# Performance work log

Measured on AMD Instinct MI355X. Metric: run time of the kernel, lower is better.

The kernel has to match this reference:

```python
import jax, jax.numpy as jnp
import numpy as np

EPS = 1e-3  # keras LayerNormalization default epsilon

def layernorm(x, gamma, beta):
    mu = jnp.mean(x, axis=-1, keepdims=True)
    var = jnp.var(x, axis=-1, keepdims=True)
    return (x - mu) * jax.lax.rsqrt(var + EPS) * gamma + beta

def setup_inputs() -> dict:
    key = jax.random.key(0)
    ks = jax.random.split(key, 20)
    B, N, T, Dimg, H = 512, 100, 14, 2048, 768
    s = lambda k, *sh: jax.random.normal(k, sh, dtype=jnp.float32) * 0.02
    return {
        "img_feat": jax.random.normal(ks[0], (B, N, Dimg), dtype=jnp.float32),
        "ques_feat": jax.random.normal(ks[1], (B, T, H), dtype=jnp.float32),
        "Wc": s(ks[2], Dimg, H), "bc": jnp.zeros((H,), jnp.float32),
        "Wq": s(ks[3], H, H),    "bq": jnp.zeros((H,), jnp.float32),
        "Wi": s(ks[4], Dimg, H), "bi": jnp.zeros((H,), jnp.float32),
        "wqa": s(ks[5], H, 1), "bqa": jnp.zeros((1,), jnp.float32),
        "wia": s(ks[6], H, 1), "bia": jnp.zeros((1,), jnp.float32),
        "g1": jnp.ones((N,), jnp.float32), "b1": jnp.zeros((N,), jnp.float32),
        "g2": jnp.ones((H,), jnp.float32), "b2": jnp.zeros((H,), jnp.float32),
        "g3": jnp.ones((T,), jnp.float32), "b3": jnp.zeros((T,), jnp.float32),
        "g4": jnp.ones((H,), jnp.float32), "b4": jnp.zeros((H,), jnp.float32),
        "g5": jnp.ones((N,), jnp.float32), "b5": jnp.zeros((N,), jnp.float32),
    }

def reference(img_feat, ques_feat, Wc, bc, Wq, bq, Wi, bi, wqa, bqa, wia, bia,
              g1, b1, g2, b2, g3, b3, g4, b4, g5, b5):
    # img_feat: [B,N,Dimg], ques_feat: [B,T,H]
    img_corr = img_feat @ Wc + bc                                   # [B,N,H]
    wm = jnp.einsum('bth,bnh->btn', ques_feat, img_corr)            # [B,T,N]
    wm = jax.nn.relu(layernorm(wm, g1, b1))
    ques_embed = ques_feat @ Wq + bq                                # [B,T,H]
    img_embed = img_feat @ Wi + bi                                  # [B,N,H]
    transform_img = jnp.einsum('btn,bnh->bth', wm, img_embed)       # [B,T,H]
    ques_atten_sum = jax.nn.relu(layernorm(transform_img + ques_embed, g2, b2))
    # dropout is identity at inference
    ques_atten = (ques_atten_sum @ wqa + bqa)[..., 0]               # [B,T]
    ques_atten = jax.nn.softmax(layernorm(ques_atten, g3, b3), axis=-1)
    transform_ques = jnp.einsum('btn,bth->bnh', wm, ques_embed)     # [B,N,H]
    img_atten_sum = jax.nn.relu(layernorm(transform_ques + img_embed, g4, b4))
    img_atten = (img_atten_sum @ wia + bia)[..., 0]                 # [B,N]
    img_atten = jax.nn.softmax(layernorm(img_atten, g5, b5), axis=-1)
    ques_atten_feat = jnp.einsum('bt,bth->bh', ques_atten, ques_feat)  # [B,H]
    img_atten_feat = jnp.einsum('bn,bnd->bd', img_atten, img_feat)     # [B,Dimg]
    return (img_atten_feat, ques_atten_feat)
```

## Files before the change

### kernel.cpp

```cpp
#include <hip/hip_runtime.h>

using f32x4     = __attribute__((ext_vector_type(4))) float;
using bf16x8    = __attribute__((ext_vector_type(8))) short;
using ushort8_t = __attribute__((ext_vector_type(8))) unsigned short;

__device__ __forceinline__ unsigned short f2bf(float f) {
    unsigned u = __builtin_bit_cast(unsigned, f);
    u += 0x7fffu + ((u >> 16) & 1u);
    return (unsigned short)(u >> 16);
}
__device__ __forceinline__ float bf2f(unsigned short h) {
    return __builtin_bit_cast(float, (unsigned)h << 16);
}

__device__ __forceinline__ float wave_sum(float v) {
#pragma unroll
    for (int off = 32; off > 0; off >>= 1) v += __shfl_xor(v, off, 64);
    return v;
}
__device__ __forceinline__ float wave_max(float v) {
#pragma unroll
    for (int off = 32; off > 0; off >>= 1) v = fmaxf(v, __shfl_xor(v, off, 64));
    return v;
}

#define GLP(p)  ((const __attribute__((address_space(1))) void*)(p))
#define LDSP(p) ((__attribute__((address_space(3))) void*)(p))

__global__ __launch_bounds__(256) void cvt_bf16(const float* __restrict__ in,
                                                unsigned short* __restrict__ out, long n8) {
    long i = (long)blockIdx.x * 256 + threadIdx.x;
    long stride = (long)gridDim.x * 256;
    for (; i < n8; i += stride) {
        const float4* p = (const float4*)(in + i * 8);
        float4 a = p[0], b = p[1];
        ushort8_t v;
        v[0] = f2bf(a.x); v[1] = f2bf(a.y); v[2] = f2bf(a.z); v[3] = f2bf(a.w);
        v[4] = f2bf(b.x); v[5] = f2bf(b.y); v[6] = f2bf(b.z); v[7] = f2bf(b.w);
        *(ushort8_t*)(out + i * 8) = v;
    }
}

__global__ void pack_w(const float* __restrict__ Wc, const float* __restrict__ Wi,
                       unsigned short* __restrict__ Wp) {
    int n = blockIdx.x, k = blockIdx.y * 256 + threadIdx.x;
    float v = (n < 768) ? Wc[(size_t)k * 768 + n] : Wi[(size_t)k * 768 + (n - 768)];
    Wp[(size_t)n * 2048 + k] = f2bf(v);
}

__global__ void pack_wq(const float* __restrict__ Wq, unsigned short* __restrict__ Wqt) {
    int n = blockIdx.x, k = blockIdx.y * 256 + threadIdx.x;
    Wqt[(size_t)n * 768 + k] = f2bf(Wq[(size_t)k * 768 + n]);
}

template <int OUTBF>
__global__ __launch_bounds__(512, 1) void gemm8(
    const unsigned short* __restrict__ A, const unsigned short* __restrict__ Bt,
    const float* __restrict__ bias0, const float* __restrict__ bias1, int nsplit,
    void* __restrict__ Cv, int N, int K, int NTN)
{
    __shared__ unsigned short LA[2][2][8192];
    __shared__ unsigned short LB[2][2][8192];
    const int tid = threadIdx.x, lane = tid & 63, wid = tid >> 6;

    int nwg = (int)gridDim.x, bid = (int)blockIdx.x;
    if ((nwg & 7) == 0) { int cpx = nwg >> 3; bid = (bid & 7) * cpx + (bid >> 3); }
    const int tn = bid % NTN, tm = bid / NTN;
    const size_t m0 = (size_t)tm * 256, n0 = (size_t)tn * 256;
    const int NT = K >> 6;
    const int NIT = NT >> 1;

    const int wr = wid >> 2, wc = wid & 3;
    const int hb = wc >> 1;
    const int fr = lane & 15, fs = lane >> 4;

    const int r0 = tid >> 3, s0 = ((tid & 7) - r0) & 7;
    const int r1 = r0 + 64,  s1 = ((tid & 7) - r1) & 7;
    const unsigned short* pA[2][2];
    const unsigned short* pB[2][2];
#pragma unroll
    for (int h = 0; h < 2; ++h) {
        pA[h][0] = A  + (m0 + h * 128 + r0) * K + s0 * 8;
        pA[h][1] = A  + (m0 + h * 128 + r1) * K + s1 * 8;
        pB[h][0] = Bt + (n0 + h * 128 + r0) * K + s0 * 8;
        pB[h][1] = Bt + (n0 + h * 128 + r1) * K + s1 * 8;
    }
    const int d0 = tid * 8, d1 = (tid + 512) * 8;

#define STG_A(h, t, B_) do { \
    __builtin_amdgcn_global_load_lds(GLP(pA[h][0] + (size_t)(t) * 64), LDSP(&LA[B_][h][d0]), 16, 0, 0); \
    __builtin_amdgcn_global_load_lds(GLP(pA[h][1] + (size_t)(t) * 64), LDSP(&LA[B_][h][d1]), 16, 0, 0); \
} while (0)
#define STG_B(h, t, B_) do { \
    __builtin_amdgcn_global_load_lds(GLP(pB[h][0] + (size_t)(t) * 64), LDSP(&LB[B_][h][d0]), 16, 0, 0); \
    __builtin_amdgcn_global_load_lds(GLP(pB[h][1] + (size_t)(t) * 64), LDSP(&LB[B_][h][d1]), 16, 0, 0); \
} while (0)

    int offA[2][4], offB[2][2];
#pragma unroll
    for (int mq = 0; mq < 2; ++mq)
#pragma unroll
        for (int mfl = 0; mfl < 4; ++mfl) {
            int r = mq * 64 + mfl * 16 + fr;
            offA[mq][mfl] = r * 64 + ((fs + r) & 7) * 8;
        }
#pragma unroll
    for (int nq = 0; nq < 2; ++nq)
#pragma unroll
        for (int nfl = 0; nfl < 2; ++nfl) {
            int r = (wc & 1) * 64 + nq * 32 + nfl * 16 + fr;
            offB[nq][nfl] = r * 64 + ((fs + r) & 7) * 8;
        }

#define LDA_SUB(B_, mq) do { \
    _Pragma("unroll") \
    for (int mfl = 0; mfl < 4; ++mfl) { \
        av[mfl][0] = *(const bf16x8*)&LA[B_][wr][offA[mq][mfl]]; \
        av[mfl][1] = *(const bf16x8*)&LA[B_][wr][offA[mq][mfl] ^ 32]; \
    } } while (0)
#define LDB_SUB(B_, nq, bv) do { \
    _Pragma("unroll") \
    for (int nfl = 0; nfl < 2; ++nfl) { \
        bv[nfl][0] = *(const bf16x8*)&LB[B_][hb][offB[nq][nfl]]; \
        bv[nfl][1] = *(const bf16x8*)&LB[B_][hb][offB[nq][nfl] ^ 32]; \
    } } while (0)
#define MMA_Q(mq, nq, bv) do { \
    _Pragma("unroll") \
    for (int ks = 0; ks < 2; ++ks) \
    _Pragma("unroll") \
    for (int mfl = 0; mfl < 4; ++mfl) \
    _Pragma("unroll") \
    for (int nfl = 0; nfl < 2; ++nfl) \
        acc[mq * 4 + mfl][nq * 2 + nfl] = __builtin_amdgcn_mfma_f32_16x16x32_bf16( \
            av[mfl][ks], bv[nfl][ks], acc[mq * 4 + mfl][nq * 2 + nfl], 0, 0, 0); \
    } while (0)
#define BAR  __builtin_amdgcn_s_barrier()
#define SCB  __builtin_amdgcn_sched_barrier(0)
#define LGKM0 do { asm volatile("s_waitcnt lgkmcnt(0)" ::: "memory"); SCB; } while (0)
#define PRIO1 __builtin_amdgcn_s_setprio(1)
#define PRIO0 __builtin_amdgcn_s_setprio(0)

    f32x4 acc[8][4];
#pragma unroll
    for (int i = 0; i < 8; ++i)
#pragma unroll
        for (int j = 0; j < 4; ++j) acc[i][j] = (f32x4){0.f, 0.f, 0.f, 0.f};

    STG_A(0, 0, 0); STG_A(1, 0, 0); STG_B(0, 0, 0); STG_B(1, 0, 0);
    STG_B(0, 1, 1); STG_B(1, 1, 1); STG_A(0, 1, 1);
    asm volatile("s_waitcnt vmcnt(6)" ::: "memory");
    SCB; BAR;

    for (int i = 0; i < NIT; ++i) {
        const int t0 = 2 * i, t1 = 2 * i + 1;
        const bool st = (i + 1 < NIT);
        bf16x8 av[4][2], bv0[2][2], bv1[2][2];

        LDA_SUB(0, 0); LDB_SUB(0, 0, bv0);
        STG_A(1, t1, 1);
        BAR; LGKM0;
        PRIO1; MMA_Q(0, 0, bv0); PRIO0;
        BAR;
        LDB_SUB(0, 1, bv1);
        BAR; LGKM0;
        PRIO1; MMA_Q(0, 1, bv1); PRIO0;
        BAR;
        LDA_SUB(0, 1);
        if (st) STG_B(0, t0 + 2, 0);
        BAR; LGKM0;
        PRIO1; MMA_Q(1, 1, bv1); PRIO0;
        BAR;
        if (st) { STG_B(1, t0 + 2, 0); STG_A(0, t0 + 2, 0); }
        BAR;
        PRIO1; MMA_Q(1, 0, bv0); PRIO0;
        if (st) asm volatile("s_waitcnt vmcnt(6)" ::: "memory");
        else    asm volatile("s_waitcnt vmcnt(0)" ::: "memory");
        SCB; BAR;
        LDA_SUB(1, 0); LDB_SUB(1, 0, bv0);
        if (st) STG_A(1, t0 + 2, 0);
        BAR; LGKM0;
        PRIO1; MMA_Q(0, 0, bv0); PRIO0;
        BAR;
        LDB_SUB(1, 1, bv1);
        BAR; LGKM0;
        PRIO1; MMA_Q(0, 1, bv1); PRIO0;
        BAR;
        LDA_SUB(1, 1);
        if (st) STG_B(0, t1 + 2, 1);
        BAR; LGKM0;
        PRIO1; MMA_Q(1, 1, bv1); PRIO0;
        BAR;
        if (st) { STG_B(1, t1 + 2, 1); STG_A(0, t1 + 2, 1); }
        BAR;
        PRIO1; MMA_Q(1, 0, bv0); PRIO0;
        if (st) asm volatile("s_waitcnt vmcnt(6)" ::: "memory");
        else    asm volatile("s_waitcnt vmcnt(0)" ::: "memory");
        SCB; BAR;
    }

#undef STG_A
#undef STG_B
#undef LDA_SUB
#undef LDB_SUB
#undef MMA_Q
#undef BAR
#undef SCB
#undef LGKM0
#undef PRIO1
#undef PRIO0

    const int wm = wr * 128, wn = wc * 64;
#pragma unroll
    for (int nf = 0; nf < 4; ++nf) {
        int col = (int)n0 + wn + nf * 16 + fr;
        float bs = (col < nsplit) ? bias0[col] : bias1[col - nsplit];
#pragma unroll
        for (int mf = 0; mf < 8; ++mf) {
            size_t rowb = m0 + wm + mf * 16 + fs * 4;
#pragma unroll
            for (int r = 0; r < 4; ++r) {
                float v = acc[mf][nf][r] + bs;
                if (OUTBF) ((unsigned short*)Cv)[(rowb + r) * N + col] = f2bf(v);
                else       ((float*)Cv)[(rowb + r) * N + col] = v;
            }
        }
    }
}

__global__ __launch_bounds__(256) void fused_kernel(
    const float* __restrict__ qf_g, const unsigned short* __restrict__ qbf,
    const float* __restrict__ qe_g, const unsigned short* __restrict__ imgCE,
    const unsigned short* __restrict__ imf_bf,
    const float* __restrict__ g1, const float* __restrict__ b1,
    const float* __restrict__ g2, const float* __restrict__ b2,
    const float* __restrict__ g3, const float* __restrict__ b3,
    const float* __restrict__ g4, const float* __restrict__ b4,
    const float* __restrict__ g5, const float* __restrict__ b5,
    const float* __restrict__ wqa, const float* __restrict__ bqa,
    const float* __restrict__ wia, const float* __restrict__ bia,
    float* __restrict__ out_i, float* __restrict__ out_q)
{
    const int b = blockIdx.x, tid = threadIdx.x, lane = tid & 63, wid = tid >> 6;
    __shared__ float buf[14 * 768];
    __shared__ float wms[14 * 100];
    __shared__ float red[4][28];
    __shared__ float mu_s[14], rs_s[14], qa_s[14], qw_s[14];
    __shared__ float mu2_s[10], rs2_s[10];
    __shared__ float ia_s[100], iw_s[100];

    {
        const ushort8_t* src = (const ushort8_t*)(qbf + (size_t)b * 14 * 768);
        for (int i = tid; i < 14 * 768 / 8; i += 256) {
            ushort8_t v = src[i];
#pragma unroll
            for (int j = 0; j < 8; ++j) buf[i * 8 + j] = bf2f(v[j]);
        }
    }
    __syncthreads();
    for (int n = wid; n < 100; n += 4) {
        const unsigned short* row = imgCE + ((size_t)b * 100 + n) * 1536;
        float r[12];
#pragma unroll
        for (int j = 0; j < 12; ++j) r[j] = bf2f(row[lane + 64 * j]);
        for (int t = 0; t < 14; ++t) {
            const float* q = buf + t * 768;
            float s = 0.f;
#pragma unroll
            for (int j = 0; j < 12; ++j) s = fmaf(r[j], q[lane + 64 * j], s);
            s = wave_sum(s);
            if (lane == 0) wms[t * 100 + n] = s;
        }
    }
    __syncthreads();
    for (int t = wid; t < 14; t += 4) {
        float x0 = wms[t * 100 + lane];
        float x1 = (lane + 64 < 100) ? wms[t * 100 + lane + 64] : 0.f;
        float s = wave_sum(x0 + x1);
        float q = wave_sum(x0 * x0 + x1 * x1);
        float mu = s * (1.f / 100.f);
        float var = q * (1.f / 100.f) - mu * mu;
        float rs = rsqrtf(var + 1e-3f);
        {
            float v = (x0 - mu) * rs * g1[lane] + b1[lane];
            wms[t * 100 + lane] = v > 0.f ? v : 0.f;
        }
        if (lane + 64 < 100) {
            float v = (x1 - mu) * rs * g1[lane + 64] + b1[lane + 64];
            wms[t * 100 + lane + 64] = v > 0.f ? v : 0.f;
        }
    }
    {
        const float4* src = (const float4*)(qe_g + (size_t)b * 14 * 768);
        for (int i = tid; i < 14 * 768 / 4; i += 256) ((float4*)buf)[i] = src[i];
    }
    __syncthreads();

    {
        float a0[14], a1[14], a2[14];
#pragma unroll
        for (int t = 0; t < 14; ++t) { a0[t] = 0.f; a1[t] = 0.f; a2[t] = 0.f; }

        const unsigned short* ie_base = imgCE + (size_t)b * 100 * 1536 + 768;
        for (int n = 0; n < 100; ++n) {
            const unsigned short* ie = ie_base + (size_t)n * 1536;
            float e0 = bf2f(ie[tid]), e1 = bf2f(ie[tid + 256]), e2 = bf2f(ie[tid + 512]);
#pragma unroll
            for (int t = 0; t < 14; ++t) {
                float w = wms[t * 100 + n];
                a0[t] = fmaf(w, e0, a0[t]); a1[t] = fmaf(w, e1, a1[t]); a2[t] = fmaf(w, e2, a2[t]);
            }
        }
#pragma unroll
        for (int t = 0; t < 14; ++t) {
            a0[t] += buf[t * 768 + tid];
            a1[t] += buf[t * 768 + tid + 256];
            a2[t] += buf[t * 768 + tid + 512];
        }
#pragma unroll
        for (int t = 0; t < 14; ++t) {
            float s = wave_sum(a0[t] + a1[t] + a2[t]);
            float q = wave_sum(a0[t] * a0[t] + a1[t] * a1[t] + a2[t] * a2[t]);
            if (lane == 0) { red[wid][t] = s; red[wid][14 + t] = q; }
        }
        __syncthreads();
        if (tid < 14) {
            float s = red[0][tid] + red[1][tid] + red[2][tid] + red[3][tid];
            float q = red[0][14 + tid] + red[1][14 + tid] + red[2][14 + tid] + red[3][14 + tid];
            float mu = s * (1.f / 768.f);
            float var = q * (1.f / 768.f) - mu * mu;
            mu_s[tid] = mu; rs_s[tid] = rsqrtf(var + 1e-3f);
        }
        __syncthreads();

        float ga = g2[tid], ba = b2[tid], gb = g2[tid + 256], bb = b2[tid + 256],
              gc = g2[tid + 512], bc_ = b2[tid + 512];
        float w0 = wqa[tid], w1 = wqa[tid + 256], w2 = wqa[tid + 512];
#pragma unroll
        for (int t = 0; t < 14; ++t) {
            float mu = mu_s[t], rs = rs_s[t];
            float v0 = fmaxf((a0[t] - mu) * rs * ga + ba, 0.f);
            float v1 = fmaxf((a1[t] - mu) * rs * gb + bb, 0.f);
            float v2 = fmaxf((a2[t] - mu) * rs * gc + bc_, 0.f);
            float p = wave_sum(v0 * w0 + v1 * w1 + v2 * w2);
            if (lane == 0) red[wid][t] = p;
        }
        __syncthreads();
        if (tid < 14) qa_s[tid] = red[0][tid] + red[1][tid] + red[2][tid] + red[3][tid] + bqa[0];
        __syncthreads();
        if (tid == 0) {
            float s = 0.f;
            for (int t = 0; t < 14; ++t) s += qa_s[t];
            float mu = s * (1.f / 14.f);
            float q = 0.f;
            for (int t = 0; t < 14; ++t) { float d = qa_s[t] - mu; q += d * d; }
            float rs = rsqrtf(q * (1.f / 14.f) + 1e-3f);
            float e[14], mx = -1e30f;
            for (int t = 0; t < 14; ++t) { e[t] = (qa_s[t] - mu) * rs * g3[t] + b3[t]; mx = fmaxf(mx, e[t]); }
            float se = 0.f;
            for (int t = 0; t < 14; ++t) { e[t] = expf(e[t] - mx); se += e[t]; }
            float inv = 1.f / se;
            for (int t = 0; t < 14; ++t) qw_s[t] = e[t] * inv;
        }
        __syncthreads();

        const float* qf = qf_g + (size_t)b * 14 * 768;
#pragma unroll
        for (int c = 0; c < 3; ++c) {
            int h = tid + c * 256;
            float o = 0.f;
#pragma unroll
            for (int t = 0; t < 14; ++t) o = fmaf(qw_s[t], qf[t * 768 + h], o);
            out_q[(size_t)b * 768 + h] = o;
        }
    }
    __syncthreads();

    {
        float g4a = g4[tid], b4a = b4[tid], g4b = g4[tid + 256], b4b = b4[tid + 256],
              g4c = g4[tid + 512], b4c = b4[tid + 512];
        float wa = wia[tid], wb = wia[tid + 256], wc_ = wia[tid + 512];

        for (int g = 0; g < 10; ++g) {
            float t0[10], t1[10], t2[10];
#pragma unroll
            for (int i = 0; i < 10; ++i) { t0[i] = 0.f; t1[i] = 0.f; t2[i] = 0.f; }
#pragma unroll
            for (int t = 0; t < 14; ++t) {
                float q0 = buf[t * 768 + tid], q1 = buf[t * 768 + tid + 256], q2 = buf[t * 768 + tid + 512];
#pragma unroll
                for (int i = 0; i < 10; ++i) {
                    float w = wms[t * 100 + g * 10 + i];
                    t0[i] = fmaf(w, q0, t0[i]); t1[i] = fmaf(w, q1, t1[i]); t2[i] = fmaf(w, q2, t2[i]);
                }
            }
#pragma unroll
            for (int i = 0; i < 10; ++i) {
                const unsigned short* ie = imgCE + ((size_t)b * 100 + g * 10 + i) * 1536 + 768;
                t0[i] += bf2f(ie[tid]); t1[i] += bf2f(ie[tid + 256]); t2[i] += bf2f(ie[tid + 512]);
                float s = wave_sum(t0[i] + t1[i] + t2[i]);
                float q = wave_sum(t0[i] * t0[i] + t1[i] * t1[i] + t2[i] * t2[i]);
                if (lane == 0) { red[wid][i] = s; red[wid][10 + i] = q; }
            }
            __syncthreads();
            if (tid < 10) {
                float s = red[0][tid] + red[1][tid] + red[2][tid] + red[3][tid];
                float q = red[0][10 + tid] + red[1][10 + tid] + red[2][10 + tid] + red[3][10 + tid];
                float mu = s * (1.f / 768.f);
                float var = q * (1.f / 768.f) - mu * mu;
                mu2_s[tid] = mu; rs2_s[tid] = rsqrtf(var + 1e-3f);
            }
            __syncthreads();
#pragma unroll
            for (int i = 0; i < 10; ++i) {
                float mu = mu2_s[i], rs = rs2_s[i];
                float v0 = fmaxf((t0[i] - mu) * rs * g4a + b4a, 0.f);
                float v1 = fmaxf((t1[i] - mu) * rs * g4b + b4b, 0.f);
                float v2 = fmaxf((t2[i] - mu) * rs * g4c + b4c, 0.f);
                float p = wave_sum(v0 * wa + v1 * wb + v2 * wc_);
                if (lane == 0) red[wid][i] = p;
            }
            __syncthreads();
            if (tid < 10) ia_s[g * 10 + tid] = red[0][tid] + red[1][tid] + red[2][tid] + red[3][tid] + bia[0];
            __syncthreads();
        }

        if (wid == 0) {
            float x0 = ia_s[lane];
            float x1 = (lane + 64 < 100) ? ia_s[lane + 64] : 0.f;
            float s = wave_sum(x0 + x1);
            float q = wave_sum(x0 * x0 + x1 * x1);
            float mu = s * 0.01f;
            float var = q * 0.01f - mu * mu;
            float rs = rsqrtf(var + 1e-3f);
            float v0 = (x0 - mu) * rs * g5[lane] + b5[lane];
            float v1 = (lane + 64 < 100) ? (x1 - mu) * rs * g5[lane + 64] + b5[lane + 64] : -1e30f;
            float mx = wave_max(fmaxf(v0, v1));
            float e0 = expf(v0 - mx);
            float e1 = (lane + 64 < 100) ? expf(v1 - mx) : 0.f;
            float se = wave_sum(e0 + e1);
            float inv = 1.f / se;
            iw_s[lane] = e0 * inv;
            if (lane + 64 < 100) iw_s[lane + 64] = e1 * inv;
        }
        __syncthreads();

        const unsigned short* imf = imf_bf + (size_t)b * 100 * 2048;
        float acc8[8];
#pragma unroll
        for (int j = 0; j < 8; ++j) acc8[j] = 0.f;
        for (int n = 0; n < 100; ++n) {
            ushort8_t v = *(const ushort8_t*)(imf + (size_t)n * 2048 + tid * 8);
            float w = iw_s[n];
#pragma unroll
            for (int j = 0; j < 8; ++j) acc8[j] = fmaf(w, bf2f(v[j]), acc8[j]);
        }
        float4* dst = (float4*)(out_i + (size_t)b * 2048);
        float4 oA = {acc8[0], acc8[1], acc8[2], acc8[3]};
        float4 oB = {acc8[4], acc8[5], acc8[6], acc8[7]};
        dst[tid * 2] = oA; dst[tid * 2 + 1] = oB;
    }
}

extern "C" void kernel_launch(void* const* d_in, const int* in_sizes, int n_in,
                              void* d_out, int out_size, void* d_ws, size_t ws_size,
                              hipStream_t stream)
{
    const float* img_feat = (const float*)d_in[0];
    const float* ques_feat = (const float*)d_in[1];
    const float* Wc = (const float*)d_in[2];
    const float* bc = (const float*)d_in[3];
    const float* Wq = (const float*)d_in[4];
    const float* bq = (const float*)d_in[5];
    const float* Wi = (const float*)d_in[6];
    const float* bi = (const float*)d_in[7];
    const float* wqa = (const float*)d_in[8];
    const float* bqa = (const float*)d_in[9];
    const float* wia = (const float*)d_in[10];
    const float* bia = (const float*)d_in[11];
    const float* g1 = (const float*)d_in[12]; const float* b1 = (const float*)d_in[13];
    const float* g2 = (const float*)d_in[14]; const float* b2 = (const float*)d_in[15];
    const float* g3 = (const float*)d_in[16]; const float* b3 = (const float*)d_in[17];
    const float* g4 = (const float*)d_in[18]; const float* b4 = (const float*)d_in[19];
    const float* g5 = (const float*)d_in[20]; const float* b5 = (const float*)d_in[21];

    const size_t SZ_WP   = 1536u * 2048u * 2u;
    const size_t SZ_WQT  = 768u * 768u * 2u;
    const size_t SZ_IMG  = 51200ull * 1536u * 2u;
    const size_t SZ_QE   = 7168u * 768u * 4u;
    const size_t SZ_WM   = 512u * 1400u * 4u;
    const size_t SZ_ABF  = 51200ull * 2048u * 2u;
    const size_t SZ_QBF  = 7168u * 768u * 2u;

    const size_t OFF_WP  = 0;
    const size_t OFF_WQT = OFF_WP + SZ_WP;
    const size_t OFF_IMG = OFF_WQT + SZ_WQT;
    const size_t OFF_QE  = OFF_IMG + SZ_IMG;
    const size_t OFF_WM  = OFF_QE + SZ_QE;
    const size_t OFF_ABF = OFF_WM + SZ_WM;
    const size_t OFF_QBF = OFF_ABF + SZ_ABF;
    const size_t NEED    = OFF_QBF + SZ_QBF;
    if (ws_size < NEED) return;

    char* ws = (char*)d_ws;
    unsigned short* Wp    = (unsigned short*)(ws + OFF_WP);
    unsigned short* Wqt   = (unsigned short*)(ws + OFF_WQT);
    unsigned short* imgCE = (unsigned short*)(ws + OFF_IMG);
    float*          qe    = (float*)(ws + OFF_QE);
    unsigned short* Abf   = (unsigned short*)(ws + OFF_ABF);
    unsigned short* Qbf   = (unsigned short*)(ws + OFF_QBF);

    float* out_img = (float*)d_out;
    float* out_q   = (float*)d_out + 512 * 2048;

    hipLaunchKernelGGL(pack_w,  dim3(1536, 8), dim3(256), 0, stream, Wc, Wi, Wp);
    hipLaunchKernelGGL(pack_wq, dim3(768, 3),  dim3(256), 0, stream, Wq, Wqt);
    hipLaunchKernelGGL(cvt_bf16, dim3(2048), dim3(256), 0, stream,
                       img_feat, Abf, (long)(51200ull * 2048u / 8u));
    hipLaunchKernelGGL(cvt_bf16, dim3(1024), dim3(256), 0, stream,
                       ques_feat, Qbf, (long)(7168u * 768u / 8u));

    hipLaunchKernelGGL(HIP_KERNEL_NAME(gemm8<1>), dim3(1200), dim3(512), 0, stream,
                       Abf, Wp, bc, bi, 768, (void*)imgCE, 1536, 2048, 6);
    hipLaunchKernelGGL(HIP_KERNEL_NAME(gemm8<0>), dim3(84), dim3(512), 0, stream,
                       Qbf, Wqt, bq, bq, 768, (void*)qe, 768, 768, 3);

    hipLaunchKernelGGL(fused_kernel, dim3(512), dim3(256), 0, stream,
                       ques_feat, Qbf, qe, imgCE, Abf,
                       g1, b1, g2, b2, g3, b3, g4, b4, g5, b5,
                       wqa, bqa, wia, bia, out_img, out_q);
}
```

Baseline: 788.2 us.

## Tile weight transposes via LDS, store ques_embed as bf16, prefetch imgCE loads

The element-wise strided pack_w/pack_wq kernels become one LDS-tiled 64x64 transpose kernel, so both the global reads and the writes are coalesced. The ques_embed GEMM now writes bf16 instead of fp32, and the fused kernel converts it on load, halving that intermediate's traffic at some precision cost. In the fused kernel, imgCE rows are software-prefetched one iteration ahead in the n loop and hoisted before the FMA loop in the g loop, to hide load latency. The extra prefetched values raise register pressure.

```diff
diff --git a/kernel.cpp b/kernel.cpp
--- a/kernel.cpp
+++ b/kernel.cpp
@@ -41,16 +41,26 @@
     }
 }
 
-__global__ void pack_w(const float* __restrict__ Wc, const float* __restrict__ Wi,
-                       unsigned short* __restrict__ Wp) {
-    int n = blockIdx.x, k = blockIdx.y * 256 + threadIdx.x;
-    float v = (n < 768) ? Wc[(size_t)k * 768 + n] : Wi[(size_t)k * 768 + (n - 768)];
-    Wp[(size_t)n * 2048 + k] = f2bf(v);
-}
-
-__global__ void pack_wq(const float* __restrict__ Wq, unsigned short* __restrict__ Wqt) {
-    int n = blockIdx.x, k = blockIdx.y * 256 + threadIdx.x;
-    Wqt[(size_t)n * 768 + k] = f2bf(Wq[(size_t)k * 768 + n]);
+__global__ __launch_bounds__(256) void pack_t(
+    const float* __restrict__ S0, const float* __restrict__ S1, int nsplit,
+    unsigned short* __restrict__ D, int K)
+{
+    __shared__ float t[64][65];
+    const int k0 = blockIdx.x * 64, n0 = blockIdx.y * 64;
+    const float* S = (n0 < nsplit) ? S0 : S1;
+    const int nb = (n0 < nsplit) ? n0 : n0 - nsplit;
+    const int c = threadIdx.x & 63, r4 = threadIdx.x >> 6;
+#pragma unroll
+    for (int it = 0; it < 16; ++it) {
+        int r = it * 4 + r4;
+        t[r][c] = S[(size_t)(k0 + r) * nsplit + nb + c];
+    }
+    __syncthreads();
+#pragma unroll
+    for (int it = 0; it < 16; ++it) {
+        int rn = it * 4 + r4;
+        D[(size_t)(n0 + rn) * K + k0 + c] = f2bf(t[c][rn]);
+    }
 }
 
 template <int OUTBF>
@@ -161,35 +171,42 @@
         BAR; LGKM0;
         PRIO1; MMA_Q(0, 0, bv0); PRIO0;
         BAR;
+
         LDB_SUB(0, 1, bv1);
         BAR; LGKM0;
         PRIO1; MMA_Q(0, 1, bv1); PRIO0;
         BAR;
+
         LDA_SUB(0, 1);
         if (st) STG_B(0, t0 + 2, 0);
         BAR; LGKM0;
         PRIO1; MMA_Q(1, 1, bv1); PRIO0;
         BAR;
+
         if (st) { STG_B(1, t0 + 2, 0); STG_A(0, t0 + 2, 0); }
         BAR;
         PRIO1; MMA_Q(1, 0, bv0); PRIO0;
         if (st) asm volatile("s_waitcnt vmcnt(6)" ::: "memory");
         else    asm volatile("s_waitcnt vmcnt(0)" ::: "memory");
         SCB; BAR;
+
         LDA_SUB(1, 0); LDB_SUB(1, 0, bv0);
         if (st) STG_A(1, t0 + 2, 0);
         BAR; LGKM0;
         PRIO1; MMA_Q(0, 0, bv0); PRIO0;
         BAR;
+
         LDB_SUB(1, 1, bv1);
         BAR; LGKM0;
         PRIO1; MMA_Q(0, 1, bv1); PRIO0;
         BAR;
+
         LDA_SUB(1, 1);
         if (st) STG_B(0, t1 + 2, 1);
         BAR; LGKM0;
         PRIO1; MMA_Q(1, 1, bv1); PRIO0;
         BAR;
+
         if (st) { STG_B(1, t1 + 2, 1); STG_A(0, t1 + 2, 1); }
         BAR;
         PRIO1; MMA_Q(1, 0, bv0); PRIO0;
@@ -229,7 +246,7 @@
 
 __global__ __launch_bounds__(256) void fused_kernel(
     const float* __restrict__ qf_g, const unsigned short* __restrict__ qbf,
-    const float* __restrict__ qe_g, const unsigned short* __restrict__ imgCE,
+    const unsigned short* __restrict__ qe_g, const unsigned short* __restrict__ imgCE,
     const unsigned short* __restrict__ imf_bf,
     const float* __restrict__ g1, const float* __restrict__ b1,
     const float* __restrict__ g2, const float* __restrict__ b2,
@@ -290,8 +307,12 @@
         }
     }
     {
-        const float4* src = (const float4*)(qe_g + (size_t)b * 14 * 768);
-        for (int i = tid; i < 14 * 768 / 4; i += 256) ((float4*)buf)[i] = src[i];
+        const ushort8_t* src = (const ushort8_t*)(qe_g + (size_t)b * 14 * 768);
+        for (int i = tid; i < 14 * 768 / 8; i += 256) {
+            ushort8_t v = src[i];
+#pragma unroll
+            for (int j = 0; j < 8; ++j) buf[i * 8 + j] = bf2f(v[j]);
+        }
     }
     __syncthreads();
 
@@ -301,9 +322,13 @@
         for (int t = 0; t < 14; ++t) { a0[t] = 0.f; a1[t] = 0.f; a2[t] = 0.f; }
 
         const unsigned short* ie_base = imgCE + (size_t)b * 100 * 1536 + 768;
+        float e0n = bf2f(ie_base[tid]), e1n = bf2f(ie_base[tid + 256]), e2n = bf2f(ie_base[tid + 512]);
         for (int n = 0; n < 100; ++n) {
-            const unsigned short* ie = ie_base + (size_t)n * 1536;
-            float e0 = bf2f(ie[tid]), e1 = bf2f(ie[tid + 256]), e2 = bf2f(ie[tid + 512]);
+            float e0 = e0n, e1 = e1n, e2 = e2n;
+            if (n < 99) {
+                const unsigned short* ie = ie_base + (size_t)(n + 1) * 1536;
+                e0n = bf2f(ie[tid]); e1n = bf2f(ie[tid + 256]); e2n = bf2f(ie[tid + 512]);
+            }
 #pragma unroll
             for (int t = 0; t < 14; ++t) {
                 float w = wms[t * 100 + n];
@@ -381,6 +406,12 @@
         float wa = wia[tid], wb = wia[tid + 256], wc_ = wia[tid + 512];
 
         for (int g = 0; g < 10; ++g) {
+            float ge0[10], ge1[10], ge2[10];
+#pragma unroll
+            for (int i = 0; i < 10; ++i) {
+                const unsigned short* ie = imgCE + ((size_t)b * 100 + g * 10 + i) * 1536 + 768;
+                ge0[i] = bf2f(ie[tid]); ge1[i] = bf2f(ie[tid + 256]); ge2[i] = bf2f(ie[tid + 512]);
+            }
             float t0[10], t1[10], t2[10];
 #pragma unroll
             for (int i = 0; i < 10; ++i) { t0[i] = 0.f; t1[i] = 0.f; t2[i] = 0.f; }
@@ -395,8 +426,7 @@
             }
 #pragma unroll
             for (int i = 0; i < 10; ++i) {
-                const unsigned short* ie = imgCE + ((size_t)b * 100 + g * 10 + i) * 1536 + 768;
-                t0[i] += bf2f(ie[tid]); t1[i] += bf2f(ie[tid + 256]); t2[i] += bf2f(ie[tid + 512]);
+                t0[i] += ge0[i]; t1[i] += ge1[i]; t2[i] += ge2[i];
                 float s = wave_sum(t0[i] + t1[i] + t2[i]);
                 float q = wave_sum(t0[i] * t0[i] + t1[i] * t1[i] + t2[i] * t2[i]);
                 if (lane == 0) { red[wid][i] = s; red[wid][10 + i] = q; }
@@ -505,15 +535,15 @@
     unsigned short* Wp    = (unsigned short*)(ws + OFF_WP);
     unsigned short* Wqt   = (unsigned short*)(ws + OFF_WQT);
     unsigned short* imgCE = (unsigned short*)(ws + OFF_IMG);
-    float*          qe    = (float*)(ws + OFF_QE);
+    unsigned short* qe    = (unsigned short*)(ws + OFF_QE);
     unsigned short* Abf   = (unsigned short*)(ws + OFF_ABF);
     unsigned short* Qbf   = (unsigned short*)(ws + OFF_QBF);
 
     float* out_img = (float*)d_out;
     float* out_q   = (float*)d_out + 512 * 2048;
 
-    hipLaunchKernelGGL(pack_w,  dim3(1536, 8), dim3(256), 0, stream, Wc, Wi, Wp);
-    hipLaunchKernelGGL(pack_wq, dim3(768, 3),  dim3(256), 0, stream, Wq, Wqt);
+    hipLaunchKernelGGL(pack_t, dim3(32, 24), dim3(256), 0, stream, Wc, Wi, 768, Wp, 2048);
+    hipLaunchKernelGGL(pack_t, dim3(12, 12), dim3(256), 0, stream, Wq, Wq, 768, Wqt, 768);
     hipLaunchKernelGGL(cvt_bf16, dim3(2048), dim3(256), 0, stream,
                        img_feat, Abf, (long)(51200ull * 2048u / 8u));
     hipLaunchKernelGGL(cvt_bf16, dim3(1024), dim3(256), 0, stream,
@@ -521,7 +551,7 @@
 
     hipLaunchKernelGGL(HIP_KERNEL_NAME(gemm8<1>), dim3(1200), dim3(512), 0, stream,
                        Abf, Wp, bc, bi, 768, (void*)imgCE, 1536, 2048, 6);
-    hipLaunchKernelGGL(HIP_KERNEL_NAME(gemm8<0>), dim3(84), dim3(512), 0, stream,
+    hipLaunchKernelGGL(HIP_KERNEL_NAME(gemm8<1>), dim3(84), dim3(512), 0, stream,
                        Qbf, Wqt, bq, bq, 768, (void*)qe, 768, 768, 3);
 
     hipLaunchKernelGGL(fused_kernel, dim3(512), dim3(256), 0, stream,
```

After: 764.5 us. 3.0% less time.
